# Optimization experiments

Hardware: AMD Instinct MI355X
Metric: run time of the kernel (lower is better)

Reference implementation:

```python
import jax, jax.numpy as jnp
import numpy as np

B, N, K = 32, 1024, 20          # graphs, points per graph, kNN neighbors
EMB = 1024                       # emb_dims
OUT = 7                          # out_channels
WS1, ST1, G1 = 52, 20, 7         # linear1 STFT-KAN: window, stride, gridsize
WS2, ST2, G2 = 197, 7, 6         # linear2 STFT-KAN
NW1 = (128 - WS1) // ST1 + 1     # 4 windows over 128-dim features
NW2 = (2 * EMB - WS2) // ST2 + 1 # 265 windows over 2048-dim features


def _window(kind, M):
    n = jnp.arange(M, dtype=jnp.float32)
    if kind == 'bartlett':
        return 1.0 - jnp.abs(2.0 * n / M - 1.0)        # periodic bartlett (torch default)
    return 0.5 * (1.0 - jnp.cos(2.0 * jnp.pi * n / M)) # periodic hann


def _stft_kan(x, coeffs, bias, gridsize, ws, stride, wtype):
    """x: [B, D]; coeffs: [2, outdim, nw, ws, gridsize]; returns [B, outdim]."""
    D = x.shape[1]
    nw = (D - ws) // stride + 1
    idx = jnp.arange(nw)[:, None] * stride + jnp.arange(ws)[None, :]  # [nw, ws]
    xw = x[:, idx] * _window(wtype, ws)                               # [B, nw, ws]
    kk = jnp.arange(1, gridsize + 1, dtype=x.dtype)
    ang = xw[..., None] * kk                                          # [B, nw, ws, g]
    y = jnp.einsum('bnwg,onwg->bo', jnp.cos(ang), coeffs[0])
    y = y + jnp.einsum('bnwg,onwg->bo', jnp.sin(ang), coeffs[1])
    return y + bias


def setup_inputs() -> dict:
    key = jax.random.key(0)
    ks = jax.random.split(key, 8)
    pos = jax.random.normal(ks[0], (B * N, 3), jnp.float32)
    batch = jnp.repeat(jnp.arange(B, dtype=jnp.int32), N)  # sorted, equal-size graphs
    # EdgeConv MLP([6,64,128]): Linear+BN+ReLU, then plain Linear
    W1 = jax.random.normal(ks[1], (6, 64), jnp.float32) * 0.3
    b1 = jnp.zeros((64,), jnp.float32)
    gamma1 = jnp.ones((64,), jnp.float32)
    beta1 = jnp.zeros((64,), jnp.float32)
    W2 = jax.random.normal(ks[2], (64, 128), jnp.float32) * 0.1
    b2 = jnp.zeros((128,), jnp.float32)
    # STFT-KAN 1 (smooth init: coeffs damped by k^2)
    k1 = np.arange(1, G1 + 1, dtype=np.float32)
    c1 = jax.random.normal(ks[3], (2, EMB, NW1, WS1, G1), jnp.float32) / (np.sqrt(NW1 * WS1) * (k1 ** 2))
    bi1 = jnp.zeros((EMB,), jnp.float32)
    # STFT-KAN 2 (non-smooth init)
    c2 = jax.random.normal(ks[4], (2, OUT, NW2, WS2, G2), jnp.float32) / (np.sqrt(NW2 * WS2) * np.sqrt(G2))
    bi2 = jnp.zeros((OUT,), jnp.float32)
    return {"pos": pos, "batch": batch, "W1": W1, "b1": b1, "gamma1": gamma1,
            "beta1": beta1, "W2": W2, "b2": b2, "c1": c1, "bi1": bi1, "c2": c2, "bi2": bi2}


def reference(pos, batch, W1, b1, gamma1, beta1, W2, b2, c1, bi1, c2, bi2):
    p = pos.reshape(B, N, 3)
    # dynamic kNN graph per batch element (exclude self)
    sq = jnp.sum(p * p, axis=-1)                                    # [B, N]
    d2 = sq[:, :, None] + sq[:, None, :] - 2.0 * jnp.einsum('bnd,bmd->bnm', p, p)
    d2 = d2 + jnp.eye(N, dtype=p.dtype) * 1e10
    _, idx = jax.lax.top_k(-d2, K)                                  # [B, N, K]
    pj = jax.vmap(lambda pts, ids: pts[ids])(p, idx)                # [B, N, K, 3]
    pi = jnp.broadcast_to(p[:, :, None, :], (B, N, K, 3))
    e = jnp.concatenate([pi, pj - pi], axis=-1)                     # [B, N, K, 6]
    # edge MLP: Linear -> BN -> ReLU -> Linear
    h = e @ W1 + b1
    mu = h.mean((0, 1, 2))
    var = h.var((0, 1, 2))
    h = gamma1 * (h - mu) * jax.lax.rsqrt(var + 1e-5) + beta1
    h = jax.nn.relu(h)
    h = h @ W2 + b2                                                 # [B, N, K, 128]
    x1 = h.max(axis=2).reshape(B * N, 128)                          # max aggregation over neighbors
    x = _stft_kan(x1, c1, bi1, G1, WS1, ST1, 'bartlett')            # [B*N, EMB]
    xg = x.reshape(B, N, EMB)
    xcat = jnp.concatenate([xg.max(axis=1), xg.mean(axis=1)], axis=-1)  # global max/mean pool
    return _stft_kan(xcat, c2, bi2, G2, WS2, ST2, 'hann')           # [B, OUT]
```

## Files before the change

kernel.cpp:

```cpp
#include <hip/hip_runtime.h>
#include <cstdint>

typedef _Float16 half8 __attribute__((ext_vector_type(8)));
typedef float f32x4 __attribute__((ext_vector_type(4)));

__device__ __forceinline__ void gload16(const void* g, void* l) {
  __builtin_amdgcn_global_load_lds(
      (const __attribute__((address_space(1))) void*)g,
      (__attribute__((address_space(3))) void*)l, 16, 0, 0);
}

__global__ __launch_bounds__(256) void knn_kernel(const float* __restrict__ pos,
                                                  int* __restrict__ nbr) {
  __shared__ float px[1024], py[1024], pz[1024], sq[1024];
  int tid = threadIdx.x;
  int b = blockIdx.x >> 8;
  const float* pg = pos + (size_t)b * 3072;
  for (int m = 0; m < 4; ++m) {
    int j = m * 256 + tid;
    float x = pg[3 * j], y = pg[3 * j + 1], z = pg[3 * j + 2];
    px[j] = x; py[j] = y; pz[j] = z; sq[j] = x * x + y * y + z * z;
  }
  __syncthreads();
  int wave = tid >> 6, lane = tid & 63;
  int n = (blockIdx.x & 255) * 4 + wave;
  float xi = px[n], yi = py[n], zi = pz[n], si = sq[n];
  float d[16];
#pragma unroll
  for (int i = 0; i < 16; ++i) {
    int j = i * 64 + lane;
    float dd = si + sq[j] - 2.0f * (xi * px[j] + yi * py[j] + zi * pz[j]);
    d[i] = (j == n) ? 1e30f : dd;
  }
  int outbase = (b * 1024 + n) * 20;
  for (int kk = 0; kk < 20; ++kk) {
    float lmin = d[0]; int lpos = 0;
#pragma unroll
    for (int i = 1; i < 16; ++i)
      if (d[i] < lmin) { lmin = d[i]; lpos = i; }
    float bv = lmin; int bi = lpos * 64 + lane;
#pragma unroll
    for (int off = 1; off < 64; off <<= 1) {
      float ov = __shfl_xor(bv, off);
      int   oi = __shfl_xor(bi, off);
      if (ov < bv || (ov == bv && oi < bi)) { bv = ov; bi = oi; }
    }
    if (lane == 0) nbr[outbase + kk] = b * 1024 + bi;
    if ((bi & 63) == lane) {
      int rp = bi >> 6;
#pragma unroll
      for (int i = 0; i < 16; ++i)
        if (i == rp) d[i] = 1e30f;
    }
  }
}

__global__ __launch_bounds__(256) void edge_stats_kernel(
    const float* __restrict__ pos, const int* __restrict__ nbr,
    const float* __restrict__ W1, const float* __restrict__ b1v,
    float* __restrict__ psum, float* __restrict__ psq) {
  __shared__ float els[256][6];
  __shared__ float w1s[384];
  __shared__ float b1s[64];
  __shared__ float red[8][64];
  int tid = threadIdx.x, bid = blockIdx.x;
  for (int f = tid; f < 384; f += 256) w1s[f] = W1[f];
  if (tid < 64) b1s[tid] = b1v[tid];
  int c = tid & 63, grp = tid >> 6;
  float s = 0.f, s2 = 0.f;
  for (int ch = 0; ch < 5; ++ch) {
    int E = bid * 1280 + ch * 256 + tid;
    int p = E / 20;
    int j = nbr[E];
    float pix = pos[3 * p], piy = pos[3 * p + 1], piz = pos[3 * p + 2];
    float e3 = pos[3 * j] - pix, e4 = pos[3 * j + 1] - piy, e5 = pos[3 * j + 2] - piz;
    __syncthreads();
    els[tid][0] = pix; els[tid][1] = piy; els[tid][2] = piz;
    els[tid][3] = e3;  els[tid][4] = e4;  els[tid][5] = e5;
    __syncthreads();
    for (int m = 0; m < 64; ++m) {
      int e = grp * 64 + m;
      float h = b1s[c];
#pragma unroll
      for (int d = 0; d < 6; ++d) h += els[e][d] * w1s[d * 64 + c];
      s += h; s2 += h * h;
    }
  }
  red[grp][c] = s;
  __syncthreads();
  red[4 + grp][c] = s2;
  __syncthreads();
  if (tid < 64) {
    float S = red[0][tid] + red[1][tid] + red[2][tid] + red[3][tid];
    float Q = red[4][tid] + red[5][tid] + red[6][tid] + red[7][tid];
    psum[bid * 64 + tid] = S;
    psq[bid * 64 + tid] = Q;
  }
}

__global__ void bn_finalize_kernel(const float* __restrict__ psum, const float* __restrict__ psq,
                                   const float* __restrict__ gamma, const float* __restrict__ beta,
                                   float* __restrict__ bns, float* __restrict__ bnh) {
  int c = threadIdx.x;
  float s = 0.f, q = 0.f;
  for (int b = 0; b < 512; ++b) { s += psum[b * 64 + c]; q += psq[b * 64 + c]; }
  const float inv = 1.0f / 655360.0f;
  float mu = s * inv;
  float var = q * inv - mu * mu;
  float sc = gamma[c] * rsqrtf(var + 1e-5f);
  bns[c] = sc;
  bnh[c] = beta[c] - mu * sc;
}

__global__ __launch_bounds__(256) void edge_mlp_kernel(
    const float* __restrict__ pos, const int* __restrict__ nbr,
    const float* __restrict__ W1, const float* __restrict__ b1v,
    const float* __restrict__ bns, const float* __restrict__ bnh,
    const float* __restrict__ W2, const float* __restrict__ b2v,
    float* __restrict__ x1) {
  __shared__ float Hl[80][65];
  __shared__ float w2s[64][128];
  __shared__ float w1s[384];
  __shared__ float b1s[64], scs[64], shs[64];
  int tid = threadIdx.x, bid = blockIdx.x;
  for (int f = tid; f < 8192; f += 256) ((float*)w2s)[f] = W2[f];
  for (int f = tid; f < 384; f += 256) w1s[f] = W1[f];
  if (tid < 64) { b1s[tid] = b1v[tid]; scs[tid] = bns[tid]; shs[tid] = bnh[tid]; }
  int d = tid & 63;
  __syncthreads();
  for (int m = 0; m < 20; ++m) {
    int flat = tid + 256 * m;
    int row = flat >> 6;
    int j = nbr[bid * 80 + row];
    int P = bid * 4 + (row / 20);
    float pix = pos[3 * P], piy = pos[3 * P + 1], piz = pos[3 * P + 2];
    float e3 = pos[3 * j] - pix, e4 = pos[3 * j + 1] - piy, e5 = pos[3 * j + 2] - piz;
    float h = b1s[d];
    h += pix * w1s[d] + piy * w1s[64 + d] + piz * w1s[128 + d]
       + e3 * w1s[192 + d] + e4 * w1s[256 + d] + e5 * w1s[320 + d];
    h = scs[d] * h + shs[d];
    Hl[row][d] = fmaxf(h, 0.f);
  }
  __syncthreads();
  int p = tid >> 6;
  int khalf = (tid >> 5) & 1;
  int cgrp = tid & 31;
  float best[4] = {-1e30f, -1e30f, -1e30f, -1e30f};
  for (int kb = khalf * 2; kb < khalf * 2 + 2; ++kb) {
    float acc[5][4] = {};
    for (int dd = 0; dd < 64; ++dd) {
      float4 wv = *(const float4*)(&w2s[dd][cgrp * 4]);
#pragma unroll
      for (int k5 = 0; k5 < 5; ++k5) {
        float hv = Hl[p * 20 + kb * 5 + k5][dd];
        acc[k5][0] += hv * wv.x; acc[k5][1] += hv * wv.y;
        acc[k5][2] += hv * wv.z; acc[k5][3] += hv * wv.w;
      }
    }
#pragma unroll
    for (int k5 = 0; k5 < 5; ++k5)
#pragma unroll
      for (int q = 0; q < 4; ++q) best[q] = fmaxf(best[q], acc[k5][q]);
  }
#pragma unroll
  for (int q = 0; q < 4; ++q) best[q] = fmaxf(best[q], __shfl_xor(best[q], 32));
  if (khalf == 0) {
    float4 o;
    o.x = best[0] + b2v[cgrp * 4 + 0];
    o.y = best[1] + b2v[cgrp * 4 + 1];
    o.z = best[2] + b2v[cgrp * 4 + 2];
    o.w = best[3] + b2v[cgrp * 4 + 3];
    *(float4*)(&x1[(bid * 4 + p) * 128 + cgrp * 4]) = o;
  }
}

__global__ void kan1_tables_kernel(int* __restrict__ dimt, float* __restrict__ wkt) {
  int j = blockIdx.x * 256 + threadIdx.x;
  if (j >= 2944) return;
  if (j >= 2912) { dimt[j] = 0; wkt[j] = 0.0f; return; }
  int r = j % 1456;
  int n = r / 364, r2 = r % 364;
  int w = r2 / 7, g = r2 % 7;
  dimt[j] = n * 20 + w;
  float bart = 1.0f - fabsf(2.0f * (float)w / 52.0f - 1.0f);
  wkt[j] = bart * (float)(g + 1);
}

__global__ void c1_to_f16_kernel(const float* __restrict__ c1, _Float16* __restrict__ Cf) {
  int L = blockIdx.x * 256 + threadIdx.x;
  if (L >= 1024 * 2944) return;
  int o = L / 2944, j = L % 2944;
  float v = 0.0f;
  if (j < 2912) {
    int t = j / 1456, r = j % 1456;
    v = c1[(size_t)(t * 1024 + o) * 1456 + r];
  }
  Cf[L] = (_Float16)v;
}

__global__ __launch_bounds__(512) void kan1_gemm_kernel(
    const float* __restrict__ x1, const _Float16* __restrict__ Cf,
    const int* __restrict__ dimt, const float* __restrict__ wkt,
    float* __restrict__ pmax, float* __restrict__ psump) {
  __shared__ __align__(16) _Float16 Asm[128 * 64];
  __shared__ __align__(16) _Float16 Bsm[256 * 64];
  __shared__ int   tdim[2][64];
  __shared__ float twk[2][64];
  __shared__ float pooled[2][2][256];
  int tid = threadIdx.x;
  int bm = blockIdx.x, bn = blockIdx.y;
  int m0 = bm << 7, n0 = bn << 8;
  int wave = tid >> 6, lane = tid & 63;
  int wr = wave >> 2, wc = wave & 3;
  int l15 = lane & 15, l4 = lane >> 4;

  if (tid < 64) { tdim[0][tid] = dimt[tid]; twk[0][tid] = wkt[tid]; }
  f32x4 acc[4][4] = {};
  __syncthreads();

  for (int t = 0; t < 46; ++t) {
    int j0 = t << 6;
#pragma unroll
    for (int i = 0; i < 4; ++i) {
      int idx = i * 512 + tid;
      int col = idx >> 3, slot = idx & 7;
      int sslot = slot ^ (col & 7);
      const _Float16* src = Cf + (size_t)(n0 + col) * 2944 + j0 + sslot * 8;
      gload16(src, (char*)Bsm + idx * 16);
    }
    if (t < 45 && tid < 64) {
      tdim[(t + 1) & 1][tid] = dimt[j0 + 64 + tid];
      twk[(t + 1) & 1][tid] = wkt[j0 + 64 + tid];
    }
    const int* td = tdim[t & 1];
    const float* tw = twk[t & 1];
#pragma unroll
    for (int rep = 0; rep < 2; ++rep) {
      int slot = tid + rep * 512;
      int r = slot >> 3, s = slot & 7;
      const float* xrow = x1 + (size_t)(m0 + r) * 128;
      int d0 = td[s * 8], d7 = td[s * 8 + 7];
      float x0 = xrow[d0], x7 = xrow[d7];
      half8 av;
#pragma unroll
      for (int e = 0; e < 8; ++e) {
        int jj = s * 8 + e;
        float xv = (td[jj] == d0) ? x0 : x7;
        float ph = (j0 + jj >= 1456) ? 1.57079632679489662f : 0.0f;
        av[e] = (_Float16)__cosf(xv * tw[jj] - ph);
      }
      *(half8*)((char*)Asm + r * 128 + ((s ^ (r & 7)) << 4)) = av;
    }
    __syncthreads();
#pragma unroll
    for (int ksub = 0; ksub < 2; ++ksub) {
      int slotk = ksub * 4 + l4;
      half8 af[4], bf[4];
#pragma unroll
      for (int mi = 0; mi < 4; ++mi) {
        int row = wr * 64 + mi * 16 + l15;
        af[mi] = *(const half8*)((char*)Asm + row * 128 + ((slotk ^ (row & 7)) << 4));
      }
#pragma unroll
      for (int ni = 0; ni < 4; ++ni) {
        int col = wc * 64 + ni * 16 + l15;
        bf[ni] = *(const half8*)((char*)Bsm + col * 128 + ((slotk ^ (col & 7)) << 4));
      }
#pragma unroll
      for (int mi = 0; mi < 4; ++mi)
#pragma unroll
        for (int ni = 0; ni < 4; ++ni)
          acc[mi][ni] = __builtin_amdgcn_mfma_f32_16x16x32_f16(af[mi], bf[ni], acc[mi][ni], 0, 0, 0);
    }
    __syncthreads();
  }

#pragma unroll
  for (int ni = 0; ni < 4; ++ni) {
    float mx = -1e30f, sm = 0.f;
#pragma unroll
    for (int mi = 0; mi < 4; ++mi)
#pragma unroll
      for (int q = 0; q < 4; ++q) {
        float v = acc[mi][ni][q];
        mx = fmaxf(mx, v); sm += v;
      }
    mx = fmaxf(mx, __shfl_xor(mx, 16)); sm += __shfl_xor(sm, 16);
    mx = fmaxf(mx, __shfl_xor(mx, 32)); sm += __shfl_xor(sm, 32);
    if (l4 == 0) {
      int col = wc * 64 + ni * 16 + l15;
      pooled[wr][0][col] = mx;
      pooled[wr][1][col] = sm;
    }
  }
  __syncthreads();
  if (tid < 256) {
    float mx = fmaxf(pooled[0][0][tid], pooled[1][0][tid]);
    float sm = pooled[0][1][tid] + pooled[1][1][tid];
    pmax[(size_t)bm * 1024 + n0 + tid] = mx;
    psump[(size_t)bm * 1024 + n0 + tid] = sm;
  }
}

__global__ void pool_reduce_kernel(const float* __restrict__ pmax, const float* __restrict__ psump,
                                   const float* __restrict__ bi1,
                                   float* __restrict__ gmax, float* __restrict__ gmean) {
  int gid = blockIdx.x * 256 + threadIdx.x;
  int b = gid >> 10, col = gid & 1023;
  float mx = -1e30f, sm = 0.f;
  for (int t = 0; t < 8; ++t) {
    mx = fmaxf(mx, pmax[(size_t)(b * 8 + t) * 1024 + col]);
    sm += psump[(size_t)(b * 8 + t) * 1024 + col];
  }
  float bias = bi1[col];
  gmax[gid] = mx + bias;
  gmean[gid] = sm * (1.0f / 1024.0f) + bias;
}

__global__ __launch_bounds__(256) void kan2_kernel(
    const float* __restrict__ gmax, const float* __restrict__ gmean,
    const float* __restrict__ c2, float* __restrict__ part) {
  __shared__ float xc[2048];
  __shared__ float hw[197];
  __shared__ float racc[7][256];
  int b = blockIdx.x, s = blockIdx.y, tid = threadIdx.x;
  for (int f = tid; f < 1024; f += 256) {
    xc[f] = gmax[b * 1024 + f];
    xc[1024 + f] = gmean[b * 1024 + f];
  }
  for (int f = tid; f < 197; f += 256)
    hw[f] = 0.5f * (1.0f - cosf(6.283185307179586f * (float)f / 197.0f));
  float acc[7] = {};
  __syncthreads();
  int qlo = (52205 * s) / 16, qhi = (52205 * (s + 1)) / 16;
  for (int q = qlo + tid; q < qhi; q += 256) {
    int n = q / 197;
    int w = q - n * 197;
    float xw = xc[n * 7 + w] * hw[w];
    float s1, c1v;
    __sincosf(xw, &s1, &c1v);
    float ckv[6], skv[6];
    {
      float ck = c1v, sk = s1;
#pragma unroll
      for (int g = 0; g < 6; ++g) {
        ckv[g] = ck; skv[g] = sk;
        float cn = ck * c1v - sk * s1;
        sk = sk * c1v + ck * s1;
        ck = cn;
      }
    }
    int base = q * 6;
#pragma unroll
    for (int o = 0; o < 7; ++o) {
      const float* pc = c2 + (size_t)o * 313230 + base;
      const float* ps = c2 + (size_t)(o + 7) * 313230 + base;
      float sc = 0.f, ss = 0.f;
#pragma unroll
      for (int g = 0; g < 6; ++g) { sc += ckv[g] * pc[g]; ss += skv[g] * ps[g]; }
      acc[o] += sc + ss;
    }
  }
#pragma unroll
  for (int o = 0; o < 7; ++o) racc[o][tid] = acc[o];
  __syncthreads();
  for (int st = 128; st >= 1; st >>= 1) {
    if (tid < st)
#pragma unroll
      for (int o = 0; o < 7; ++o) racc[o][tid] += racc[o][tid + st];
    __syncthreads();
  }
  if (tid < 7) part[(b * 16 + s) * 7 + tid] = racc[tid][0];
}

__global__ void kan2_reduce_kernel(const float* __restrict__ part, const float* __restrict__ bi2,
                                   float* __restrict__ out) {
  int i = threadIdx.x;
  if (i >= 224) return;
  int b = i / 7, o = i % 7;
  float s = 0.f;
  for (int t = 0; t < 16; ++t) s += part[(b * 16 + t) * 7 + o];
  out[b * 7 + o] = s + bi2[o];
}

extern "C" void kernel_launch(void* const* d_in, const int* in_sizes, int n_in,
                              void* d_out, int out_size, void* d_ws, size_t ws_size,
                              hipStream_t stream) {
  const float* pos    = (const float*)d_in[0];
  const float* W1     = (const float*)d_in[2];
  const float* b1     = (const float*)d_in[3];
  const float* gamma1 = (const float*)d_in[4];
  const float* beta1  = (const float*)d_in[5];
  const float* W2     = (const float*)d_in[6];
  const float* b2     = (const float*)d_in[7];
  const float* c1     = (const float*)d_in[8];
  const float* bi1    = (const float*)d_in[9];
  const float* c2     = (const float*)d_in[10];
  const float* bi2    = (const float*)d_in[11];
  float* out = (float*)d_out;
  char* ws = (char*)d_ws;

  int*      nbr   = (int*)     (ws + 0);
  float*    x1    = (float*)   (ws + 2621440);
  _Float16* Cf    = (_Float16*)(ws + 19398656);
  int*      dimt  = (int*)     (ws + 25427968);
  float*    wkt   = (float*)   (ws + 25439744);
  float*    psum  = (float*)   (ws + 25451520);
  float*    psq   = (float*)   (ws + 25582592);
  float*    bns   = (float*)   (ws + 25713664);
  float*    bnh   = (float*)   (ws + 25713920);
  float*    pmax  = (float*)   (ws + 25714176);
  float*    psump = (float*)   (ws + 26762752);
  float*    gmax  = (float*)   (ws + 27811328);
  float*    gmean = (float*)   (ws + 27942400);
  float*    part  = (float*)   (ws + 28073472);
  if (ws_size < 28087808) return;

  knn_kernel<<<8192, 256, 0, stream>>>(pos, nbr);
  kan1_tables_kernel<<<12, 256, 0, stream>>>(dimt, wkt);
  c1_to_f16_kernel<<<11776, 256, 0, stream>>>(c1, Cf);
  edge_stats_kernel<<<512, 256, 0, stream>>>(pos, nbr, W1, b1, psum, psq);
  bn_finalize_kernel<<<1, 64, 0, stream>>>(psum, psq, gamma1, beta1, bns, bnh);
  edge_mlp_kernel<<<8192, 256, 0, stream>>>(pos, nbr, W1, b1, bns, bnh, W2, b2, x1);
  kan1_gemm_kernel<<<dim3(256, 4), 512, 0, stream>>>(x1, Cf, dimt, wkt, pmax, psump);
  pool_reduce_kernel<<<128, 256, 0, stream>>>(pmax, psump, bi1, gmax, gmean);
  kan2_kernel<<<dim3(32, 16), 256, 0, stream>>>(gmax, gmean, c2, part);
  kan2_reduce_kernel<<<1, 256, 0, stream>>>(part, bi2, out);
}
```

Measured before the change: 722.0 us.

## Use split-f16 MFMA for edge MLP second layer and retile KAN1 GEMM

The edge MLP's second linear layer moves from scalar FP32 FMAs to MFMA, with both activations and weights split into hi/lo f16 pairs and three MFMAs per tile to keep near-FP32 accuracy. Results are staged in LDS before the per-point max over neighbours. Separately, the KAN1 GEMM goes from 128x256 tiles with 512 threads to 128x128 tiles with 256 threads and launch bounds of 4 blocks, doubling the grid. This trades more cosine recomputation of the A tile for smaller LDS use and higher occupancy.

```diff
diff --git a/kernel.cpp b/kernel.cpp
--- a/kernel.cpp
+++ b/kernel.cpp
@@ -118,19 +118,34 @@
     const float* __restrict__ bns, const float* __restrict__ bnh,
     const float* __restrict__ W2, const float* __restrict__ b2v,
     float* __restrict__ x1) {
-  __shared__ float Hl[80][65];
-  __shared__ float w2s[64][128];
+  __shared__ __align__(16) char elds[53248];
+  _Float16* Ah = (_Float16*)(elds);
+  _Float16* Al = (_Float16*)(elds + 10240);
+  _Float16* Bh = (_Float16*)(elds + 20480);
+  _Float16* Bl = (_Float16*)(elds + 36864);
+  float* outb = (float*)elds;
   __shared__ float w1s[384];
   __shared__ float b1s[64], scs[64], shs[64];
   int tid = threadIdx.x, bid = blockIdx.x;
-  for (int f = tid; f < 8192; f += 256) ((float*)w2s)[f] = W2[f];
   for (int f = tid; f < 384; f += 256) w1s[f] = W1[f];
   if (tid < 64) { b1s[tid] = b1v[tid]; scs[tid] = bns[tid]; shs[tid] = bnh[tid]; }
-  int d = tid & 63;
-  __syncthreads();
+#pragma unroll
+  for (int i = 0; i < 32; ++i) {
+    int flat = tid + 256 * i;
+    int dd = flat >> 7, c = flat & 127;
+    float v = W2[flat];
+    _Float16 hi = (_Float16)v;
+    _Float16 lo = (_Float16)(v - (float)hi);
+    int byte = c * 128 + ((((dd >> 3) ^ (c & 7))) << 4) + (dd & 7) * 2;
+    *(_Float16*)((char*)Bh + byte) = hi;
+    *(_Float16*)((char*)Bl + byte) = lo;
+  }
+  __syncthreads();
+#pragma unroll
   for (int m = 0; m < 20; ++m) {
     int flat = tid + 256 * m;
     int row = flat >> 6;
+    int d = flat & 63;
     int j = nbr[bid * 80 + row];
     int P = bid * 4 + (row / 20);
     float pix = pos[3 * P], piy = pos[3 * P + 1], piz = pos[3 * P + 2];
@@ -139,38 +154,63 @@
     h += pix * w1s[d] + piy * w1s[64 + d] + piz * w1s[128 + d]
        + e3 * w1s[192 + d] + e4 * w1s[256 + d] + e5 * w1s[320 + d];
     h = scs[d] * h + shs[d];
-    Hl[row][d] = fmaxf(h, 0.f);
-  }
-  __syncthreads();
-  int p = tid >> 6;
-  int khalf = (tid >> 5) & 1;
-  int cgrp = tid & 31;
-  float best[4] = {-1e30f, -1e30f, -1e30f, -1e30f};
-  for (int kb = khalf * 2; kb < khalf * 2 + 2; ++kb) {
-    float acc[5][4] = {};
-    for (int dd = 0; dd < 64; ++dd) {
-      float4 wv = *(const float4*)(&w2s[dd][cgrp * 4]);
-#pragma unroll
-      for (int k5 = 0; k5 < 5; ++k5) {
-        float hv = Hl[p * 20 + kb * 5 + k5][dd];
-        acc[k5][0] += hv * wv.x; acc[k5][1] += hv * wv.y;
-        acc[k5][2] += hv * wv.z; acc[k5][3] += hv * wv.w;
-      }
-    }
-#pragma unroll
-    for (int k5 = 0; k5 < 5; ++k5)
-#pragma unroll
-      for (int q = 0; q < 4; ++q) best[q] = fmaxf(best[q], acc[k5][q]);
-  }
-#pragma unroll
-  for (int q = 0; q < 4; ++q) best[q] = fmaxf(best[q], __shfl_xor(best[q], 32));
-  if (khalf == 0) {
-    float4 o;
-    o.x = best[0] + b2v[cgrp * 4 + 0];
-    o.y = best[1] + b2v[cgrp * 4 + 1];
-    o.z = best[2] + b2v[cgrp * 4 + 2];
-    o.w = best[3] + b2v[cgrp * 4 + 3];
-    *(float4*)(&x1[(bid * 4 + p) * 128 + cgrp * 4]) = o;
+    h = fmaxf(h, 0.f);
+    _Float16 hi = (_Float16)h;
+    _Float16 lo = (_Float16)(h - (float)hi);
+    int byte = row * 128 + ((((d >> 3) ^ (row & 7))) << 4) + (d & 7) * 2;
+    *(_Float16*)((char*)Ah + byte) = hi;
+    *(_Float16*)((char*)Al + byte) = lo;
+  }
+  __syncthreads();
+  int wave = tid >> 6, lane = tid & 63;
+  int l15 = lane & 15, l4 = lane >> 4;
+  f32x4 acc[5][2] = {};
+#pragma unroll
+  for (int ks = 0; ks < 2; ++ks) {
+    int slotk = ks * 4 + l4;
+    half8 bfh[2], bfl[2];
+#pragma unroll
+    for (int ci = 0; ci < 2; ++ci) {
+      int col = (wave * 2 + ci) * 16 + l15;
+      int byte = col * 128 + ((slotk ^ (col & 7)) << 4);
+      bfh[ci] = *(const half8*)((char*)Bh + byte);
+      bfl[ci] = *(const half8*)((char*)Bl + byte);
+    }
+#pragma unroll
+    for (int rt = 0; rt < 5; ++rt) {
+      int row = rt * 16 + l15;
+      int byte = row * 128 + ((slotk ^ (row & 7)) << 4);
+      half8 ah = *(const half8*)((char*)Ah + byte);
+      half8 al = *(const half8*)((char*)Al + byte);
+#pragma unroll
+      for (int ci = 0; ci < 2; ++ci) {
+        acc[rt][ci] = __builtin_amdgcn_mfma_f32_16x16x32_f16(ah, bfh[ci], acc[rt][ci], 0, 0, 0);
+        acc[rt][ci] = __builtin_amdgcn_mfma_f32_16x16x32_f16(ah, bfl[ci], acc[rt][ci], 0, 0, 0);
+        acc[rt][ci] = __builtin_amdgcn_mfma_f32_16x16x32_f16(al, bfh[ci], acc[rt][ci], 0, 0, 0);
+      }
+    }
+  }
+  __syncthreads();
+#pragma unroll
+  for (int rt = 0; rt < 5; ++rt)
+#pragma unroll
+    for (int ci = 0; ci < 2; ++ci) {
+      int col = (wave * 2 + ci) * 16 + l15;
+#pragma unroll
+      for (int q = 0; q < 4; ++q) {
+        int row = rt * 16 + l4 * 4 + q;
+        outb[row * 129 + col] = acc[rt][ci][q];
+      }
+    }
+  __syncthreads();
+#pragma unroll
+  for (int r = 0; r < 2; ++r) {
+    int it = tid + 256 * r;
+    int p = it >> 7, c = it & 127;
+    float mx = -1e30f;
+#pragma unroll
+    for (int e = 0; e < 20; ++e) mx = fmaxf(mx, outb[(p * 20 + e) * 129 + c]);
+    x1[((size_t)bid * 4 + p) * 128 + c] = mx + b2v[c];
   }
 }
 
@@ -198,20 +238,19 @@
   Cf[L] = (_Float16)v;
 }
 
-__global__ __launch_bounds__(512) void kan1_gemm_kernel(
+__global__ __launch_bounds__(256, 4) void kan1_gemm_kernel(
     const float* __restrict__ x1, const _Float16* __restrict__ Cf,
     const int* __restrict__ dimt, const float* __restrict__ wkt,
     float* __restrict__ pmax, float* __restrict__ psump) {
   __shared__ __align__(16) _Float16 Asm[128 * 64];
-  __shared__ __align__(16) _Float16 Bsm[256 * 64];
+  __shared__ __align__(16) _Float16 Bsm[128 * 64];
   __shared__ int   tdim[2][64];
   __shared__ float twk[2][64];
-  __shared__ float pooled[2][2][256];
   int tid = threadIdx.x;
   int bm = blockIdx.x, bn = blockIdx.y;
-  int m0 = bm << 7, n0 = bn << 8;
+  int m0 = bm << 7, n0 = bn << 7;
   int wave = tid >> 6, lane = tid & 63;
-  int wr = wave >> 2, wc = wave & 3;
+  int wr = wave >> 1, wc = wave & 1;
   int l15 = lane & 15, l4 = lane >> 4;
 
   if (tid < 64) { tdim[0][tid] = dimt[tid]; twk[0][tid] = wkt[tid]; }
@@ -222,7 +261,7 @@
     int j0 = t << 6;
 #pragma unroll
     for (int i = 0; i < 4; ++i) {
-      int idx = i * 512 + tid;
+      int idx = i * 256 + tid;
       int col = idx >> 3, slot = idx & 7;
       int sslot = slot ^ (col & 7);
       const _Float16* src = Cf + (size_t)(n0 + col) * 2944 + j0 + sslot * 8;
@@ -235,8 +274,8 @@
     const int* td = tdim[t & 1];
     const float* tw = twk[t & 1];
 #pragma unroll
-    for (int rep = 0; rep < 2; ++rep) {
-      int slot = tid + rep * 512;
+    for (int rep = 0; rep < 4; ++rep) {
+      int slot = tid + rep * 256;
       int r = slot >> 3, s = slot & 7;
       const float* xrow = x1 + (size_t)(m0 + r) * 128;
       int d0 = td[s * 8], d7 = td[s * 8 + 7];
@@ -255,26 +294,25 @@
 #pragma unroll
     for (int ksub = 0; ksub < 2; ++ksub) {
       int slotk = ksub * 4 + l4;
-      half8 af[4], bf[4];
-#pragma unroll
-      for (int mi = 0; mi < 4; ++mi) {
-        int row = wr * 64 + mi * 16 + l15;
-        af[mi] = *(const half8*)((char*)Asm + row * 128 + ((slotk ^ (row & 7)) << 4));
-      }
+      half8 bf[4];
 #pragma unroll
       for (int ni = 0; ni < 4; ++ni) {
         int col = wc * 64 + ni * 16 + l15;
         bf[ni] = *(const half8*)((char*)Bsm + col * 128 + ((slotk ^ (col & 7)) << 4));
       }
 #pragma unroll
-      for (int mi = 0; mi < 4; ++mi)
+      for (int mi = 0; mi < 4; ++mi) {
+        int row = wr * 64 + mi * 16 + l15;
+        half8 af = *(const half8*)((char*)Asm + row * 128 + ((slotk ^ (row & 7)) << 4));
 #pragma unroll
         for (int ni = 0; ni < 4; ++ni)
-          acc[mi][ni] = __builtin_amdgcn_mfma_f32_16x16x32_f16(af[mi], bf[ni], acc[mi][ni], 0, 0, 0);
+          acc[mi][ni] = __builtin_amdgcn_mfma_f32_16x16x32_f16(af, bf[ni], acc[mi][ni], 0, 0, 0);
+      }
     }
     __syncthreads();
   }
 
+  float* pooled = (float*)Bsm;
 #pragma unroll
   for (int ni = 0; ni < 4; ++ni) {
     float mx = -1e30f, sm = 0.f;
@@ -289,14 +327,14 @@
     mx = fmaxf(mx, __shfl_xor(mx, 32)); sm += __shfl_xor(sm, 32);
     if (l4 == 0) {
       int col = wc * 64 + ni * 16 + l15;
-      pooled[wr][0][col] = mx;
-      pooled[wr][1][col] = sm;
-    }
-  }
-  __syncthreads();
-  if (tid < 256) {
-    float mx = fmaxf(pooled[0][0][tid], pooled[1][0][tid]);
-    float sm = pooled[0][1][tid] + pooled[1][1][tid];
+      pooled[(wr * 2 + 0) * 128 + col] = mx;
+      pooled[(wr * 2 + 1) * 128 + col] = sm;
+    }
+  }
+  __syncthreads();
+  if (tid < 128) {
+    float mx = fmaxf(pooled[tid], pooled[2 * 128 + tid]);
+    float sm = pooled[128 + tid] + pooled[3 * 128 + tid];
     pmax[(size_t)bm * 1024 + n0 + tid] = mx;
     psump[(size_t)bm * 1024 + n0 + tid] = sm;
   }
@@ -422,7 +460,7 @@
   edge_stats_kernel<<<512, 256, 0, stream>>>(pos, nbr, W1, b1, psum, psq);
   bn_finalize_kernel<<<1, 64, 0, stream>>>(psum, psq, gamma1, beta1, bns, bnh);
   edge_mlp_kernel<<<8192, 256, 0, stream>>>(pos, nbr, W1, b1, bns, bnh, W2, b2, x1);
-  kan1_gemm_kernel<<<dim3(256, 4), 512, 0, stream>>>(x1, Cf, dimt, wkt, pmax, psump);
+  kan1_gemm_kernel<<<dim3(256, 8), 256, 0, stream>>>(x1, Cf, dimt, wkt, pmax, psump);
   pool_reduce_kernel<<<128, 256, 0, stream>>>(pmax, psump, bi1, gmax, gmean);
   kan2_kernel<<<dim3(32, 16), 256, 0, stream>>>(gmax, gmean, c2, part);
   kan2_reduce_kernel<<<1, 256, 0, stream>>>(part, bi2, out);
```

Result: faster. 660.8 us (-8.5%).
